# Kernel tuning notes

Hardware: AMD Instinct MI355X
Metric: run time of the kernel (lower is better)

## Reference

```python
import jax, jax.numpy as jnp
from jax import lax
import numpy as np

N, BITS, NCLS = 2048, 64, 100
LAMBDA = 1.0
ALPHA = 1.0


def setup_inputs() -> dict:
    key = jax.random.key(0)
    ku, kl = jax.random.split(key)
    u = jax.random.normal(ku, (N, BITS), dtype=jnp.float32)
    labels = jax.random.randint(kl, (N,), 0, NCLS)
    y = jax.nn.one_hot(labels, NCLS, dtype=jnp.float32)  # [N, C]
    return {"u": u, "y": y}


def reference(u, y):
    # inner_product[i, j] = <u_i, u_j>;  s[i, j] = (y_i . y_j > 0)
    ip = u @ u.T                      # [N, N]
    s = (y @ y.T) > 0                 # [N, N] bool

    def step(carry, xs):
        tot, cnt = carry
        ip_row, s_row = xs            # [N], [N]
        pos = s_row
        neg = ~s_row
        # triple[p, n] = ip[p] - ip[n] - ALPHA, clamped like the original
        T = jnp.clip(ip_row[:, None] - ip_row[None, :] - ALPHA, -100.0, 50.0)
        # -(T - log(1 + exp(T))) = softplus(T) - T
        L = jax.nn.softplus(T) - T    # [N, N]
        pm = (pos[:, None] & neg[None, :]).astype(L.dtype)
        npairs = pm.sum()
        valid = (pos.sum() > 0) & (neg.sum() > 0)
        row_loss = jnp.where(valid, (L * pm).sum() / jnp.maximum(npairs, 1.0), 0.0)
        return (tot + row_loss, cnt + valid.astype(jnp.float32)), None

    (tot, cnt), _ = lax.scan(step, (jnp.float32(0.0), jnp.float32(0.0)), (ip, s))
    loss1 = jnp.where(cnt > 0, tot / jnp.maximum(cnt, 1.0), 0.0)
    loss2 = LAMBDA * jnp.mean((u - jnp.sign(u)) ** 2)
    return loss1 + loss2
```

## Files before the change

kernel.cpp:

```cpp
#include <hip/hip_runtime.h>
#include <hip/hip_bf16.h>
#include <math.h>

#define NROWS 2048
#define BITS  64
#define NCLS  100
#define ALPHA_C  1.0f
#define LAMBDA_C 1.0f
#define ECLAMP   1.0e9f
#define NPMAX    64
#define EPS      20

typedef __bf16 bf16x8 __attribute__((ext_vector_type(8)));
typedef float  floatx4 __attribute__((ext_vector_type(4)));


__device__ __forceinline__ float block_reduce_sum(float v, float* wsum) {
    __syncthreads();
    #pragma unroll
    for (int off = 32; off > 0; off >>= 1) v += __shfl_down(v, off);
    int tid = threadIdx.x;
    if ((tid & 63) == 0) wsum[tid >> 6] = v;
    __syncthreads();
    float r = 0.f;
    if (tid == 0) {
        #pragma unroll
        for (int w = 0; w < 4; ++w) r += wsum[w];
    }
    return r;
}

__device__ __forceinline__ float softplus_mt(float T) {
    return fmaxf(-T, 0.f) + __logf(1.f + __expf(-fabsf(T)));
}


__global__ __launch_bounds__(256) void prep_kernel(const float* __restrict__ u,
                                                   const float* __restrict__ y,
                                                   unsigned short* __restrict__ ub,
                                                   unsigned char* __restrict__ lab8,
                                                   float* __restrict__ qp,
                                                   float* __restrict__ rl) {
    const int tid = threadIdx.x;
    if (blockIdx.x < 64) {
        __shared__ float wsum[4];
        const int base = blockIdx.x * 2048 + tid * 8;
        float4 v0 = *(const float4*)(u + base);
        float4 v1 = *(const float4*)(u + base + 4);
        float vv[8] = {v0.x, v0.y, v0.z, v0.w, v1.x, v1.y, v1.z, v1.w};
        unsigned short ob[8];
        float q = 0.f;
        #pragma unroll
        for (int m = 0; m < 8; ++m) {
            const float v = vv[m];
            const float sg = (v > 0.f) ? 1.f : ((v < 0.f) ? -1.f : 0.f);
            const float d = v - sg;
            q = fmaf(d, d, q);
            __hip_bfloat16 h = __float2bfloat16(v);
            ob[m] = *reinterpret_cast<unsigned short*>(&h);
        }
        *(uint4*)(ub + base) = *(const uint4*)ob;
        float t = block_reduce_sum(q, wsum);
        if (tid == 0) qp[blockIdx.x] = t;
    } else {
        const int bi = blockIdx.x - 64;
        if (tid == 0) ((float4*)rl)[bi] = make_float4(0.f, 0.f, 0.f, 0.f);
        const int row = bi * 4 + (tid >> 6);
        const int lane = tid & 63;
        const float* yr = y + (size_t)row * NCLS;
        float v0 = yr[lane];
        float v1 = (lane < NCLS - 64) ? yr[lane + 64] : 0.f;
        unsigned long long m0 = __ballot(v0 > 0.5f);
        unsigned long long m1 = __ballot(v1 > 0.5f);
        if (lane == 0) {
            int c = m0 ? (__ffsll(m0) - 1) : (m1 ? 64 + __ffsll(m1) - 1 : 0);
            lab8[row] = (unsigned char)c;
        }
    }
}

__global__ __launch_bounds__(256) void posk_kernel(const float* __restrict__ u,
                                                   const unsigned char* __restrict__ lab8,
                                                   float* __restrict__ Ep,
                                                   int* __restrict__ npg) {
    __shared__ unsigned char labL[NROWS];
    __shared__ float uloc[4][BITS];
    __shared__ int   lstJ[4][NPMAX];
    const int tid = threadIdx.x;
    const int wave = tid >> 6;
    const int lane = tid & 63;
    const int row = blockIdx.x * 4 + wave;

    ((uint2*)labL)[tid] = ((const uint2*)lab8)[tid];
    uloc[wave][lane] = u[(size_t)row * BITS + lane];
    __syncthreads();

    const int ci = labL[row];
    int np = 0;
    const unsigned long long mylt = (lane == 63) ? ~0ull >> 1
                                                 : ((1ull << (lane + 1)) - 1) >> 1;
    #pragma unroll 4
    for (int m = 0; m < NROWS / 64; ++m) {
        const int j = m * 64 + lane;
        const bool match = (labL[j] == ci);
        unsigned long long bal = __ballot(match);
        if (bal) {
            if (match) {
                const unsigned long long below = (lane == 0) ? 0ull : (bal << (64 - lane));
                const int slot = np + __popcll(below);
                if (slot < NPMAX) lstJ[wave][slot] = j;
            }
            np += __popcll(bal);
        }
    }
    const int npc = (np < NPMAX) ? np : NPMAX;

    float val = 0.f;
    if (lane < npc) {
        const int j = lstJ[wave][lane];
        const float4* uj4 = (const float4*)(u + (size_t)j * BITS);
        float s0 = 0.f, s1 = 0.f, s2 = 0.f, s3 = 0.f;
        #pragma unroll
        for (int kk = 0; kk < BITS / 4; ++kk) {
            float4 vj = uj4[kk];
            s0 = fmaf(vj.x, uloc[wave][4 * kk + 0], s0);
            s1 = fmaf(vj.y, uloc[wave][4 * kk + 1], s1);
            s2 = fmaf(vj.z, uloc[wave][4 * kk + 2], s2);
            s3 = fmaf(vj.w, uloc[wave][4 * kk + 3], s3);
        }
        val = fminf(__expf(-((s0 + s1) + (s2 + s3))), ECLAMP);
    }
    Ep[(size_t)row * NPMAX + lane] = val;
    if (lane == 0) npg[row] = np;
}

__global__ __launch_bounds__(256, 4) void evalj2_kernel(const unsigned short* __restrict__ ub,
                                                        const unsigned char* __restrict__ lab8,
                                                        const float* __restrict__ Ep,
                                                        const int* __restrict__ npg,
                                                        float* __restrict__ rl) {
    __shared__ unsigned char labL[NROWS];
    __shared__ float epT[NPMAX][EPS];
    __shared__ int np16[16];
    __shared__ float wsum[16][4];

    const int tid  = threadIdx.x;
    const int wave = tid >> 6;
    const int lane = tid & 63;
    const int rsel = lane & 15;
    const int quad = lane >> 4;
    const int koff = quad * 8;
    const int i0    = (blockIdx.x >> 3) * 16;
    const int jbase = (blockIdx.x & 7) * 256;

    ((uint2*)labL)[tid] = ((const uint2*)lab8)[tid];
    #pragma unroll
    for (int it = 0; it < 4; ++it) {
        const int idx = tid + it * 256;
        const int r = idx >> 6, k = idx & 63;
        epT[k][r] = Ep[(size_t)(i0 + r) * NPMAX + k];
    }
    if (tid < 16) np16[tid] = npg[i0 + tid];

    uint4 a0r = *(const uint4*)(ub + (size_t)(i0 + rsel) * BITS + koff);
    uint4 a1r = *(const uint4*)(ub + (size_t)(i0 + rsel) * BITS + 32 + koff);
    bf16x8 A0 = __builtin_bit_cast(bf16x8, a0r);
    bf16x8 A1 = __builtin_bit_cast(bf16x8, a1r);

    float Eb[4][4];
    int colj[4];
    #pragma unroll
    for (int t = 0; t < 4; ++t) {
        const int j0 = jbase + (wave * 4 + t) * 16;
        const int jr = j0 + rsel;
        colj[t] = jr;
        uint4 b0r = *(const uint4*)(ub + (size_t)jr * BITS + koff);
        uint4 b1r = *(const uint4*)(ub + (size_t)jr * BITS + 32 + koff);
        bf16x8 B0 = __builtin_bit_cast(bf16x8, b0r);
        bf16x8 B1 = __builtin_bit_cast(bf16x8, b1r);
        floatx4 c = {0.f, 0.f, 0.f, 0.f};
        c = __builtin_amdgcn_mfma_f32_16x16x32_bf16(A0, B0, c, 0, 0, 0);
        c = __builtin_amdgcn_mfma_f32_16x16x32_bf16(A1, B1, c, 0, 0, 0);
        #pragma unroll
        for (int r = 0; r < 4; ++r) {
            const int rowLab = labL[i0 + 4 * quad + r];
            const int colLab = labL[jr];
            Eb[t][r] = (colLab == rowLab) ? 0.f
                                          : fminf(__expf(c[r] + ALPHA_C), ECLAMP);
        }
    }
    __syncthreads();

    int npmx = 0;
    #pragma unroll
    for (int r = 0; r < 16; ++r) {
        int n = np16[r]; n = (n > NPMAX) ? NPMAX : n;
        npmx = (n > npmx) ? n : npmx;
    }
    const int npr = (npmx + 1) & ~1;

    float s[4] = {0.f, 0.f, 0.f, 0.f};
    for (int k = 0; k < npr; k += 2) {
        const float4 e0 = *(const float4*)(&epT[k][4 * quad]);
        const float4 e1 = *(const float4*)(&epT[k + 1][4 * quad]);
        const float e0v[4] = {e0.x, e0.y, e0.z, e0.w};
        const float e1v[4] = {e1.x, e1.y, e1.z, e1.w};
        #pragma unroll
        for (int t = 0; t < 4; ++t) {
            #pragma unroll
            for (int r = 0; r < 4; ++r) {
                const float q0 = Eb[t][r];
                const float f = fmaf(q0, e0v[r], 1.f);
                const float g = fmaf(q0, e1v[r], 1.f);
                s[r] += __log2f(f * g);
            }
        }
    }

    #pragma unroll
    for (int r = 0; r < 4; ++r) {
        #pragma unroll
        for (int off = 1; off < 16; off <<= 1) s[r] += __shfl_xor(s[r], off);
    }
    if (rsel == 0) {
        #pragma unroll
        for (int r = 0; r < 4; ++r) wsum[4 * quad + r][wave] = s[r];
    }
    __syncthreads();
    if (tid < 16) {
        const float ln2 = 0.6931471805599453f;
        const float tot = ((wsum[tid][0] + wsum[tid][1]) +
                           (wsum[tid][2] + wsum[tid][3])) * ln2;
        atomicAdd(&rl[i0 + tid], tot);
    }
}

__global__ __launch_bounds__(256) void finalize3_kernel(const float* __restrict__ rl,
                                                        const int* __restrict__ npg,
                                                        const float* __restrict__ qp,
                                                        float* __restrict__ out) {
    __shared__ float wsum[4];
    const int tid = threadIdx.x;
    float t = 0.f, v = 0.f;
    for (int row = tid; row < NROWS; row += 256) {
        const int np = npg[row];
        const int nneg = NROWS - np;
        const int valid = (np > 0 && nneg > 0) ? 1 : 0;
        t += valid ? (rl[row] / fmaxf((float)np * (float)nneg, 1.f)) : 0.f;
        v += (float)valid;
    }
    float q = (tid < 64) ? qp[tid] : 0.f;
    float tt = block_reduce_sum(t, wsum);
    float vv = block_reduce_sum(v, wsum);
    float qq = block_reduce_sum(q, wsum);
    if (tid == 0) {
        const float loss1 = (vv > 0.f) ? (tt / fmaxf(vv, 1.f)) : 0.f;
        const float loss2 = LAMBDA_C * (qq / (float)(NROWS * BITS));
        out[0] = loss1 + loss2;
    }
}


__global__ __launch_bounds__(256) void labels_only_kernel(const float* __restrict__ y,
                                                          int* __restrict__ labels) {
    const int tid = threadIdx.x;
    const int row = blockIdx.x * 4 + (tid >> 6);
    const int lane = tid & 63;
    const float* yr = y + (size_t)row * NCLS;
    float v0 = yr[lane];
    float v1 = (lane < NCLS - 64) ? yr[lane + 64] : 0.f;
    unsigned long long m0 = __ballot(v0 > 0.5f);
    unsigned long long m1 = __ballot(v1 > 0.5f);
    if (lane == 0) {
        int c = m0 ? (__ffsll(m0) - 1) : (m1 ? 64 + __ffsll(m1) - 1 : 0);
        labels[row] = c;
    }
}

__global__ __launch_bounds__(256) void row_loss_kernel(const float* __restrict__ u,
                                                       const int* __restrict__ labels,
                                                       float* __restrict__ acc) {
    __shared__ float a[NROWS];
    __shared__ float apv[NROWS];
    __shared__ int lab[NROWS];
    __shared__ float ui[BITS];
    __shared__ int npos_s;
    __shared__ float wsum[4];

    const int i = blockIdx.x;
    const int tid = threadIdx.x;

    if (tid < BITS) ui[tid] = u[(size_t)i * BITS + tid];
    if (tid == 0) npos_s = 0;
    __syncthreads();

    #pragma unroll
    for (int m = 0; m < NROWS / 256; ++m) {
        const int j = tid + m * 256;
        const float4* uj = (const float4*)(u + (size_t)j * BITS);
        float s0 = 0.f, s1 = 0.f, s2 = 0.f, s3 = 0.f;
        #pragma unroll
        for (int q = 0; q < BITS / 4; ++q) {
            float4 v = uj[q];
            s0 = fmaf(v.x, ui[4 * q + 0], s0);
            s1 = fmaf(v.y, ui[4 * q + 1], s1);
            s2 = fmaf(v.z, ui[4 * q + 2], s2);
            s3 = fmaf(v.w, ui[4 * q + 3], s3);
        }
        a[j] = (s0 + s1) + (s2 + s3);
        lab[j] = labels[j];
    }
    __syncthreads();

    const int c = lab[i];
    #pragma unroll
    for (int m = 0; m < NROWS / 256; ++m) {
        const int j = tid + m * 256;
        if (lab[j] == c) { int k = atomicAdd(&npos_s, 1); apv[k] = a[j]; }
    }
    __syncthreads();
    const int npos = npos_s;
    const int nneg = NROWS - npos;

    float b[NROWS / 256];
    #pragma unroll
    for (int m = 0; m < NROWS / 256; ++m) {
        const int j = tid + m * 256;
        b[m] = (lab[j] != c) ? (a[j] + ALPHA_C) : -3.0e38f;
    }

    float lsum = 0.f;
    for (int k = 0; k < npos; ++k) {
        const float apk = apv[k];
        #pragma unroll
        for (int m = 0; m < NROWS / 256; ++m) lsum += softplus_mt(apk - b[m]);
    }

    float tot = block_reduce_sum(lsum, wsum);
    if (tid == 0) {
        const int valid = (npos > 0 && nneg > 0) ? 1 : 0;
        const float npairs = fmaxf((float)npos * (float)nneg, 1.f);
        const float rlv = valid ? (tot / npairs) : 0.f;
        atomicAdd(&acc[0], rlv);
        atomicAdd(&acc[1], (float)valid);
    }
}

__global__ __launch_bounds__(256) void quant_kernel(const float* __restrict__ u,
                                                    float* __restrict__ acc) {
    __shared__ float wsum[4];
    const int stride = gridDim.x * 256;
    float s = 0.f;
    for (int t = blockIdx.x * 256 + threadIdx.x; t < NROWS * BITS; t += stride) {
        float v = u[t];
        float sg = (v > 0.f) ? 1.f : ((v < 0.f) ? -1.f : 0.f);
        float d = v - sg;
        s = fmaf(d, d, s);
    }
    float tot = block_reduce_sum(s, wsum);
    if (threadIdx.x == 0) atomicAdd(&acc[2], tot);
}

__global__ void finalize_kernel(const float* __restrict__ acc,
                                float* __restrict__ out) {
    const float tot = acc[0], cnt = acc[1], q = acc[2];
    const float loss1 = (cnt > 0.f) ? (tot / fmaxf(cnt, 1.f)) : 0.f;
    const float loss2 = LAMBDA_C * (q / (float)(NROWS * BITS));
    out[0] = loss1 + loss2;
}


extern "C" void kernel_launch(void* const* d_in, const int* in_sizes, int n_in,
                              void* d_out, int out_size, void* d_ws, size_t ws_size,
                              hipStream_t stream) {
    const float* u = (const float*)d_in[0];
    const float* y = (const float*)d_in[1];
    float* out = (float*)d_out;

    unsigned char* lab8 = (unsigned char*)d_ws;
    float* rl  = (float*)((char*)d_ws + 8192);
    int*   npg = (int*)((char*)d_ws + 16384);
    float* qp  = (float*)((char*)d_ws + 24576);
    float* Ep  = (float*)((char*)d_ws + 32768);
    unsigned short* ub = (unsigned short*)((char*)d_ws + 557056);
    const size_t NEED = 557056 + (size_t)NROWS * BITS * sizeof(unsigned short);

    if (ws_size >= NEED) {
        prep_kernel<<<576, 256, 0, stream>>>(u, y, ub, lab8, qp, rl);
        posk_kernel<<<512, 256, 0, stream>>>(u, lab8, Ep, npg);
        evalj2_kernel<<<1024, 256, 0, stream>>>(ub, lab8, Ep, npg, rl);
        finalize3_kernel<<<1, 256, 0, stream>>>(rl, npg, qp, out);
    } else {
        float* acc2 = (float*)d_ws;
        int*   lab2 = (int*)((char*)d_ws + 256);
        hipMemsetAsync(d_ws, 0, 256, stream);
        labels_only_kernel<<<512, 256, 0, stream>>>(y, lab2);
        row_loss_kernel<<<NROWS, 256, 0, stream>>>(u, lab2, acc2);
        quant_kernel<<<64, 256, 0, stream>>>(u, acc2);
        finalize_kernel<<<1, 1, 0, stream>>>(acc2, out);
    }
}
```

Before: 83.76 us.

## Fuse positive-pair, pairwise-eval and finalize kernels into one with last-block reduction

```diff
diff --git a/kernel.cpp b/kernel.cpp
--- a/kernel.cpp
+++ b/kernel.cpp
@@ -40,7 +40,8 @@
                                                    unsigned short* __restrict__ ub,
                                                    unsigned char* __restrict__ lab8,
                                                    float* __restrict__ qp,
-                                                   float* __restrict__ rl) {
+                                                   float* __restrict__ rl,
+                                                   unsigned int* __restrict__ done) {
     const int tid = threadIdx.x;
     if (blockIdx.x < 64) {
         __shared__ float wsum[4];
@@ -64,6 +65,7 @@
         if (tid == 0) qp[blockIdx.x] = t;
     } else {
         const int bi = blockIdx.x - 64;
+        if (bi == 0 && tid == 0) *done = 0u;
         if (tid == 0) ((float4*)rl)[bi] = make_float4(0.f, 0.f, 0.f, 0.f);
         const int row = bi * 4 + (tid >> 6);
         const int lane = tid & 63;
@@ -79,70 +81,24 @@
     }
 }
 
-__global__ __launch_bounds__(256) void posk_kernel(const float* __restrict__ u,
-                                                   const unsigned char* __restrict__ lab8,
-                                                   float* __restrict__ Ep,
-                                                   int* __restrict__ npg) {
+__global__ __launch_bounds__(512, 4) void fused_kernel(const float* __restrict__ u,
+                                                       const unsigned short* __restrict__ ub,
+                                                       const unsigned char* __restrict__ lab8,
+                                                       const float* __restrict__ qp,
+                                                       float* __restrict__ rl,
+                                                       unsigned int* __restrict__ done,
+                                                       float* __restrict__ out) {
     __shared__ unsigned char labL[NROWS];
-    __shared__ float uloc[4][BITS];
-    __shared__ int   lstJ[4][NPMAX];
-    const int tid = threadIdx.x;
-    const int wave = tid >> 6;
-    const int lane = tid & 63;
-    const int row = blockIdx.x * 4 + wave;
-
-    ((uint2*)labL)[tid] = ((const uint2*)lab8)[tid];
-    uloc[wave][lane] = u[(size_t)row * BITS + lane];
-    __syncthreads();
-
-    const int ci = labL[row];
-    int np = 0;
-    const unsigned long long mylt = (lane == 63) ? ~0ull >> 1
-                                                 : ((1ull << (lane + 1)) - 1) >> 1;
-    #pragma unroll 4
-    for (int m = 0; m < NROWS / 64; ++m) {
-        const int j = m * 64 + lane;
-        const bool match = (labL[j] == ci);
-        unsigned long long bal = __ballot(match);
-        if (bal) {
-            if (match) {
-                const unsigned long long below = (lane == 0) ? 0ull : (bal << (64 - lane));
-                const int slot = np + __popcll(below);
-                if (slot < NPMAX) lstJ[wave][slot] = j;
-            }
-            np += __popcll(bal);
-        }
-    }
-    const int npc = (np < NPMAX) ? np : NPMAX;
-
-    float val = 0.f;
-    if (lane < npc) {
-        const int j = lstJ[wave][lane];
-        const float4* uj4 = (const float4*)(u + (size_t)j * BITS);
-        float s0 = 0.f, s1 = 0.f, s2 = 0.f, s3 = 0.f;
-        #pragma unroll
-        for (int kk = 0; kk < BITS / 4; ++kk) {
-            float4 vj = uj4[kk];
-            s0 = fmaf(vj.x, uloc[wave][4 * kk + 0], s0);
-            s1 = fmaf(vj.y, uloc[wave][4 * kk + 1], s1);
-            s2 = fmaf(vj.z, uloc[wave][4 * kk + 2], s2);
-            s3 = fmaf(vj.w, uloc[wave][4 * kk + 3], s3);
-        }
-        val = fminf(__expf(-((s0 + s1) + (s2 + s3))), ECLAMP);
-    }
-    Ep[(size_t)row * NPMAX + lane] = val;
-    if (lane == 0) npg[row] = np;
-}
-
-__global__ __launch_bounds__(256, 4) void evalj2_kernel(const unsigned short* __restrict__ ub,
-                                                        const unsigned char* __restrict__ lab8,
-                                                        const float* __restrict__ Ep,
-                                                        const int* __restrict__ npg,
-                                                        float* __restrict__ rl) {
-    __shared__ unsigned char labL[NROWS];
+    __shared__ float uloc[16][BITS];
     __shared__ float epT[NPMAX][EPS];
-    __shared__ int np16[16];
-    __shared__ float wsum[16][4];
+    __shared__ int   clsIdx[NROWS];
+    __shared__ int   ccnt[NCLS];
+    __shared__ int   cofs[NCLS];
+    __shared__ int   cpos[NCLS];
+    __shared__ int   np16[16];
+    __shared__ float wsum[16][8];
+    __shared__ float red8[8];
+    __shared__ int   lastflag;
 
     const int tid  = threadIdx.x;
     const int wave = tid >> 6;
@@ -150,44 +106,88 @@
     const int rsel = lane & 15;
     const int quad = lane >> 4;
     const int koff = quad * 8;
-    const int i0    = (blockIdx.x >> 3) * 16;
-    const int jbase = (blockIdx.x & 7) * 256;
-
-    ((uint2*)labL)[tid] = ((const uint2*)lab8)[tid];
-    #pragma unroll
-    for (int it = 0; it < 4; ++it) {
-        const int idx = tid + it * 256;
-        const int r = idx >> 6, k = idx & 63;
-        epT[k][r] = Ep[(size_t)(i0 + r) * NPMAX + k];
-    }
-    if (tid < 16) np16[tid] = npg[i0 + tid];
+    const int i0    = (blockIdx.x >> 2) * 16;
+    const int jbase = (blockIdx.x & 3) * 512;
+
+    ((unsigned int*)labL)[tid] = ((const unsigned int*)lab8)[tid];
+    ((float2*)uloc)[tid] = ((const float2*)(u + (size_t)i0 * BITS))[tid];
+    if (tid < NCLS) ccnt[tid] = 0;
 
     uint4 a0r = *(const uint4*)(ub + (size_t)(i0 + rsel) * BITS + koff);
     uint4 a1r = *(const uint4*)(ub + (size_t)(i0 + rsel) * BITS + 32 + koff);
+    uint4 b0r[4], b1r[4];
+    #pragma unroll
+    for (int t = 0; t < 4; ++t) {
+        const int jr = jbase + (wave * 4 + t) * 16 + rsel;
+        b0r[t] = *(const uint4*)(ub + (size_t)jr * BITS + koff);
+        b1r[t] = *(const uint4*)(ub + (size_t)jr * BITS + 32 + koff);
+    }
+    __syncthreads();
+
+    #pragma unroll
+    for (int m = 0; m < 4; ++m) atomicAdd(&ccnt[labL[tid + m * 512]], 1);
+    __syncthreads();
+    if (tid == 0) {
+        int run = 0;
+        for (int c = 0; c < NCLS; ++c) { cofs[c] = run; run += ccnt[c]; }
+    }
+    __syncthreads();
+    if (tid < NCLS) cpos[tid] = cofs[tid];
+    __syncthreads();
+    #pragma unroll
+    for (int m = 0; m < 4; ++m) {
+        const int j = tid + m * 512;
+        const int p = atomicAdd(&cpos[labL[j]], 1);
+        clsIdx[p] = j;
+    }
+
     bf16x8 A0 = __builtin_bit_cast(bf16x8, a0r);
     bf16x8 A1 = __builtin_bit_cast(bf16x8, a1r);
-
     float Eb[4][4];
-    int colj[4];
     #pragma unroll
     for (int t = 0; t < 4; ++t) {
-        const int j0 = jbase + (wave * 4 + t) * 16;
-        const int jr = j0 + rsel;
-        colj[t] = jr;
-        uint4 b0r = *(const uint4*)(ub + (size_t)jr * BITS + koff);
-        uint4 b1r = *(const uint4*)(ub + (size_t)jr * BITS + 32 + koff);
-        bf16x8 B0 = __builtin_bit_cast(bf16x8, b0r);
-        bf16x8 B1 = __builtin_bit_cast(bf16x8, b1r);
-        floatx4 c = {0.f, 0.f, 0.f, 0.f};
-        c = __builtin_amdgcn_mfma_f32_16x16x32_bf16(A0, B0, c, 0, 0, 0);
-        c = __builtin_amdgcn_mfma_f32_16x16x32_bf16(A1, B1, c, 0, 0, 0);
+        bf16x8 B0 = __builtin_bit_cast(bf16x8, b0r[t]);
+        bf16x8 B1 = __builtin_bit_cast(bf16x8, b1r[t]);
+        floatx4 cacc = {0.f, 0.f, 0.f, 0.f};
+        cacc = __builtin_amdgcn_mfma_f32_16x16x32_bf16(A0, B0, cacc, 0, 0, 0);
+        cacc = __builtin_amdgcn_mfma_f32_16x16x32_bf16(A1, B1, cacc, 0, 0, 0);
+        const int jr = jbase + (wave * 4 + t) * 16 + rsel;
+        const int colLab = labL[jr];
         #pragma unroll
         for (int r = 0; r < 4; ++r) {
             const int rowLab = labL[i0 + 4 * quad + r];
-            const int colLab = labL[jr];
             Eb[t][r] = (colLab == rowLab) ? 0.f
-                                          : fminf(__expf(c[r] + ALPHA_C), ECLAMP);
-        }
+                                          : fminf(__expf(cacc[r] + ALPHA_C), ECLAMP);
+        }
+    }
+    __syncthreads();
+
+    #pragma unroll
+    for (int s2 = 0; s2 < 2; ++s2) {
+        const int r16 = wave * 2 + s2;
+        const int ci  = labL[i0 + r16];
+        const int np  = ccnt[ci];
+        const int base = cofs[ci];
+        const int npc = (np < NPMAX) ? np : NPMAX;
+        float val = 0.f;
+        if (lane < npc) {
+            const int j = clsIdx[base + lane];
+            const float4* uj4 = (const float4*)(u + (size_t)j * BITS);
+            const float4* ui4 = (const float4*)(&uloc[r16][0]);
+            float s0 = 0.f, s1 = 0.f, s2v = 0.f, s3 = 0.f;
+            #pragma unroll
+            for (int kk = 0; kk < BITS / 4; ++kk) {
+                float4 vj = uj4[kk];
+                float4 vi = ui4[kk];
+                s0 = fmaf(vj.x, vi.x, s0);
+                s1 = fmaf(vj.y, vi.y, s1);
+                s2v = fmaf(vj.z, vi.z, s2v);
+                s3 = fmaf(vj.w, vi.w, s3);
+            }
+            val = fminf(__expf(-((s0 + s1) + (s2v + s3))), ECLAMP);
+        }
+        epT[lane][r16] = val;
+        if (lane == 0) np16[r16] = np;
     }
     __syncthreads();
 
@@ -229,34 +229,54 @@
     __syncthreads();
     if (tid < 16) {
         const float ln2 = 0.6931471805599453f;
-        const float tot = ((wsum[tid][0] + wsum[tid][1]) +
-                           (wsum[tid][2] + wsum[tid][3])) * ln2;
+        const float tot = (((wsum[tid][0] + wsum[tid][1]) +
+                            (wsum[tid][2] + wsum[tid][3])) +
+                           ((wsum[tid][4] + wsum[tid][5]) +
+                            (wsum[tid][6] + wsum[tid][7]))) * ln2;
         atomicAdd(&rl[i0 + tid], tot);
     }
-}
-
-__global__ __launch_bounds__(256) void finalize3_kernel(const float* __restrict__ rl,
-                                                        const int* __restrict__ npg,
-                                                        const float* __restrict__ qp,
-                                                        float* __restrict__ out) {
-    __shared__ float wsum[4];
-    const int tid = threadIdx.x;
-    float t = 0.f, v = 0.f;
-    for (int row = tid; row < NROWS; row += 256) {
-        const int np = npg[row];
-        const int nneg = NROWS - np;
-        const int valid = (np > 0 && nneg > 0) ? 1 : 0;
-        t += valid ? (rl[row] / fmaxf((float)np * (float)nneg, 1.f)) : 0.f;
-        v += (float)valid;
-    }
-    float q = (tid < 64) ? qp[tid] : 0.f;
-    float tt = block_reduce_sum(t, wsum);
-    float vv = block_reduce_sum(v, wsum);
-    float qq = block_reduce_sum(q, wsum);
+    __syncthreads();
+
     if (tid == 0) {
-        const float loss1 = (vv > 0.f) ? (tt / fmaxf(vv, 1.f)) : 0.f;
-        const float loss2 = LAMBDA_C * (qq / (float)(NROWS * BITS));
-        out[0] = loss1 + loss2;
+        __threadfence();
+        const unsigned int old = atomicAdd(done, 1u);
+        lastflag = (old == 511u) ? 1 : 0;
+    }
+    __syncthreads();
+    if (lastflag) {
+        float tsum = 0.f, vsum = 0.f;
+        for (int row = tid; row < NROWS; row += 512) {
+            const float rv = atomicAdd(&rl[row], 0.0f);
+            const int np = ccnt[labL[row]];
+            const int nn = NROWS - np;
+            const int valid = (np > 0 && nn > 0) ? 1 : 0;
+            tsum += valid ? (rv / fmaxf((float)np * (float)nn, 1.f)) : 0.f;
+            vsum += (float)valid;
+        }
+        float q = (tid < 64) ? qp[tid] : 0.f;
+
+        float vals[3] = {tsum, vsum, q};
+        float outv[3];
+        #pragma unroll
+        for (int m = 0; m < 3; ++m) {
+            float v = vals[m];
+            #pragma unroll
+            for (int off = 32; off > 0; off >>= 1) v += __shfl_down(v, off);
+            if (lane == 0) red8[wave] = v;
+            __syncthreads();
+            float r = 0.f;
+            if (tid == 0) {
+                #pragma unroll
+                for (int w = 0; w < 8; ++w) r += red8[w];
+            }
+            __syncthreads();
+            outv[m] = r;
+        }
+        if (tid == 0) {
+            const float loss1 = (outv[1] > 0.f) ? (outv[0] / fmaxf(outv[1], 1.f)) : 0.f;
+            const float loss2 = LAMBDA_C * (outv[2] / (float)(NROWS * BITS));
+            out[0] = loss1 + loss2;
+        }
     }
 }
 
@@ -378,18 +398,15 @@
     float* out = (float*)d_out;
 
     unsigned char* lab8 = (unsigned char*)d_ws;
-    float* rl  = (float*)((char*)d_ws + 8192);
-    int*   npg = (int*)((char*)d_ws + 16384);
-    float* qp  = (float*)((char*)d_ws + 24576);
-    float* Ep  = (float*)((char*)d_ws + 32768);
-    unsigned short* ub = (unsigned short*)((char*)d_ws + 557056);
-    const size_t NEED = 557056 + (size_t)NROWS * BITS * sizeof(unsigned short);
+    unsigned int* done = (unsigned int*)((char*)d_ws + 4096);
+    float* rl = (float*)((char*)d_ws + 8192);
+    float* qp = (float*)((char*)d_ws + 16384);
+    unsigned short* ub = (unsigned short*)((char*)d_ws + 24576);
+    const size_t NEED = 24576 + (size_t)NROWS * BITS * sizeof(unsigned short);
 
     if (ws_size >= NEED) {
-        prep_kernel<<<576, 256, 0, stream>>>(u, y, ub, lab8, qp, rl);
-        posk_kernel<<<512, 256, 0, stream>>>(u, lab8, Ep, npg);
-        evalj2_kernel<<<1024, 256, 0, stream>>>(ub, lab8, Ep, npg, rl);
-        finalize3_kernel<<<1, 256, 0, stream>>>(rl, npg, qp, out);
+        prep_kernel<<<576, 256, 0, stream>>>(u, y, ub, lab8, qp, rl, done);
+        fused_kernel<<<512, 512, 0, stream>>>(u, ub, lab8, qp, rl, done, out);
     } else {
         float* acc2 = (float*)d_ws;
         int*   lab2 = (int*)((char*)d_ws + 256);
```

Measured after the change: 84.46 us. About the same (+0.8%).
